# Kernel optimization log

Hardware: AMD Instinct MI355X
Metric: run time of the kernel (lower is better)

The kernel has to match this reference:

```python
import jax, jax.numpy as jnp
import numpy as np

NTYPE = 4
NWAVE = 8
NORBIT = 128
NIPSIN = 3
CUTOFF = 5.0
NEIGH = 64
NB = 32
NATOM = 256
NPAIR_PER = NATOM * NEIGH  # pairs per molecule

# index_para: [0, 1,1,1, 2,...x9] -> length 1 + 3 + 9 = 13
INDEX_PARA = np.concatenate([np.zeros(1, np.int32)] + [np.full(3 ** i, i, np.int32) for i in range(1, NIPSIN)])
NPARA = INDEX_PARA.shape[0]  # 13


def setup_inputs() -> dict:
    key = jax.random.key(0)
    ks = jax.random.split(key, 12)
    cart = jax.random.normal(ks[0], (NB, NATOM, 3), dtype=jnp.float32)
    numatoms = jnp.full((NB,), NATOM, dtype=jnp.int32)
    species = jax.random.randint(ks[1], (NB * NATOM,), 0, NTYPE, dtype=jnp.int32)
    atom_index = jax.random.randint(ks[2], (2, NB, NPAIR_PER), 0, NATOM, dtype=jnp.int32)
    # small nonzero shifts so no pair has exactly zero distance
    shifts = 0.1 * jax.random.normal(ks[3], (NB, NPAIR_PER, 3), dtype=jnp.float32)
    rs = jax.random.uniform(ks[4], (NTYPE, NWAVE), dtype=jnp.float32) * CUTOFF
    inta = -jnp.abs(jax.random.normal(ks[5], (NTYPE, NWAVE), dtype=jnp.float32))
    params = jnp.ones((NTYPE, NWAVE), dtype=jnp.float32) / float(NEIGH)
    hyper = 0.1 * jax.random.normal(ks[6], (NIPSIN, NWAVE, NORBIT), dtype=jnp.float32)
    oc_w0 = 0.05 * jax.random.normal(ks[7], (NORBIT, NWAVE), dtype=jnp.float32)
    oc_e0 = 0.05 * jax.random.normal(ks[8], (NTYPE, NWAVE), dtype=jnp.float32)
    oc_w1 = 0.05 * jax.random.normal(ks[9], (NORBIT, NWAVE), dtype=jnp.float32)
    oc_e1 = 0.05 * jax.random.normal(ks[10], (NTYPE, NWAVE), dtype=jnp.float32)
    return {"cart": cart, "shifts": shifts, "rs": rs, "inta": inta, "params": params,
            "hyper": hyper, "oc_w0": oc_w0, "oc_e0": oc_e0, "oc_w1": oc_w1, "oc_e1": oc_e1,
            "numatoms": numatoms, "species": species, "atom_index": atom_index}


def _angular(dist_vec, f_cut):
    # dist_vec: (N, 3), f_cut: (N,) -> (NPARA, N)
    dv = dist_vec.T  # (3, N)
    ang = f_cut[None, :]  # (1, N)
    parts = [ang]
    for _ in range(1, NIPSIN):
        ang = (ang[:, None, :] * dv[None, :, :]).reshape(-1, ang.shape[-1])
        parts.append(ang)
    return jnp.concatenate(parts, axis=0)  # (13, N)


def reference(cart, shifts, rs, inta, params, hyper, oc_w0, oc_e0, oc_w1, oc_e1,
              numatoms, species, atom_index):
    nbatch, numatom, _ = cart.shape
    totnatom = nbatch * numatom
    # global pair indices: per-molecule neighbor indices + molecule offset
    offsets = jnp.arange(nbatch, dtype=atom_index.dtype) * numatom  # (nbatch,)
    idx12 = (atom_index + offsets[None, :, None]).reshape(2, -1)  # (2, Npair)
    cart_ = cart.reshape(-1, 3)  # (totnatom, 3)
    dist_vec = cart_[idx12[0]] - cart_[idx12[1]] + shifts.reshape(-1, 3)  # (Npair, 3)
    distances = jnp.linalg.norm(dist_vec, axis=-1)  # (Npair,)
    f_cut = jnp.square(0.5 * jnp.cos(distances * (jnp.pi / CUTOFF)) + 0.5)
    sp_pair = species[idx12[1]]  # (Npair,)
    # radial gaussian: exp(inta * (d - rs)^2), per-pair type gather
    radial = jnp.exp(inta[sp_pair] * jnp.square(distances[:, None] - rs[sp_pair]))  # (Npair, nwave)
    ang = _angular(dist_vec, f_cut)  # (NPARA, Npair)
    # orbital[i, j, k] = ang[j, i] * radial[i, k]
    orbital = ang.T[:, :, None] * radial[:, None, :]  # (Npair, NPARA, nwave)
    hyper_exp = hyper[jnp.asarray(INDEX_PARA)]  # (NPARA, nwave, norbit)

    def obtain(orb_coeff):
        worbital = orbital * orb_coeff[idx12[1]][:, None, :]  # gather + scale
        sum_worbital = jax.ops.segment_sum(worbital, idx12[0], num_segments=totnatom)
        hyper_worbital = jnp.einsum('ijk,jkm->ijm', sum_worbital, hyper_exp)
        return jnp.sum(jnp.square(hyper_worbital), axis=1)  # (totnatom, norbit)

    orb_coeff = params[species]  # (totnatom, nwave)
    density = obtain(orb_coeff)
    for w, e in ((oc_w0, oc_e0), (oc_w1, oc_e1)):
        orb_coeff = orb_coeff + jnp.tanh(density @ w + e[species])
        density = obtain(orb_coeff)
    return density
```

## Files before the change

kernel.cpp:

```cpp
#include <hip/hip_runtime.h>
#include <math.h>

#define NTYPE   4
#define NWAVE   8
#define NORBIT  128
#define NEIGH   64
#define NB      32
#define NATOM   256
#define NPP     (NATOM * NEIGH)
#define NPAIR   (NB * NPP)
#define TOTATOM (NB * NATOM)
#define NPARA   13
#define CAP     128

__device__ __forceinline__ float fast_tanh(float x) {
    float ax = fabsf(x);
    float e  = __expf(-2.0f * ax);
    float r  = (1.0f - e) / (1.0f + e);
    return copysignf(r, x);
}

__global__ __launch_bounds__(256) void k_scatter(
    const int* __restrict__ atom_index, const float* __restrict__ cart,
    const float* __restrict__ shifts, const int* __restrict__ species,
    const float* __restrict__ params, const float* __restrict__ rs,
    const float* __restrict__ inta,
    int* __restrict__ cnt, float4* __restrict__ rec,
    float4* __restrict__ radfc, float* __restrict__ coeffA)
{
    const int bl = blockIdx.x, t = threadIdx.x;
    const int b = bl >> 5, c = bl & 31;
    __shared__ float cx[NATOM], cy[NATOM], cz[NATOM];
    __shared__ int   spl[NATOM];
    __shared__ float lrs[NTYPE * NWAVE], lin[NTYPE * NWAVE];
    if (t < NTYPE * NWAVE) { lrs[t] = rs[t]; lin[t] = inta[t]; }
    const int ag = b * NATOM + t;
    cx[t] = cart[ag * 3 + 0];
    cy[t] = cart[ag * 3 + 1];
    cz[t] = cart[ag * 3 + 2];
    spl[t] = species[ag];
    __syncthreads();

    if (c == 0) {
        int sp = spl[t];
#pragma unroll
        for (int w = 0; w < NWAVE; w++) coeffA[ag * NWAVE + w] = params[sp * NWAVE + w];
    }

    const int base = b * NPP + c * 512;
#pragma unroll
    for (int k = 0; k < 2; k++) {
        int p = base + t + k * 256;
        int i = atom_index[p];
        int j = atom_index[NPAIR + p];
        float dx = cx[i] - cx[j] + shifts[p * 3 + 0];
        float dy = cy[i] - cy[j] + shifts[p * 3 + 1];
        float dz = cz[i] - cz[j] + shifts[p * 3 + 2];
        int sp = spl[j];
        float d  = sqrtf(dx * dx + dy * dy + dz * dz);
        float co = __cosf(d * 0.62831853071795864769f);
        float fc = 0.5f * co + 0.5f;
        fc = fc * fc;
        int ig = b * NATOM + i;
        int pos = atomicAdd(&cnt[ig], 1);
        if (pos < CAP) {
            size_t s = (size_t)ig * CAP + pos;
            rec[s] = make_float4(dx, dy, dz, __int_as_float(b * NATOM + j));
            float f[NWAVE];
#pragma unroll
            for (int w = 0; w < NWAVE; w++) {
                float dr = d - lrs[sp * NWAVE + w];
                f[w] = fc * __expf(lin[sp * NWAVE + w] * dr * dr);
            }
            radfc[s * 2 + 0] = make_float4(f[0], f[1], f[2], f[3]);
            radfc[s * 2 + 1] = make_float4(f[4], f[5], f[6], f[7]);
        }
    }
}

__global__ __launch_bounds__(256) void k_pass(
    const float4* __restrict__ rec, const float* __restrict__ radfc,
    const int* __restrict__ cnt, const float* __restrict__ coeff_in,
    const float* __restrict__ hyper, const float* __restrict__ W,
    const float* __restrict__ E, const int* __restrict__ species,
    float* __restrict__ coeff_out, float* __restrict__ density_out, int mode)
{
    const int t = threadIdx.x;
    const int lane = t & 63, wv = t >> 6;
    const int pl = lane >> 3, w = lane & 7;
    const int a = blockIdx.x * 4 + wv;
    __shared__ float lds_S[4][NWAVE * 16];

    int n = cnt[a];
    if (n > CAP) n = CAP;
    const float4* ra = rec + (size_t)a * CAP;
    const float*  rf = radfc + (size_t)a * CAP * 8;

    float S[NPARA];
#pragma unroll
    for (int k = 0; k < NPARA; k++) S[k] = 0.0f;

    int idx = pl;
    float4 r = ra[idx];
    float  f = rf[idx * 8 + w];
    while (idx < n) {
        float4 rn = ra[idx + 8];
        float  fn = rf[(idx + 8) * 8 + w];
        int j = __float_as_int(r.w);
        float cj = coeff_in[j * NWAVE + w];
        float q = f * cj;
        S[0] += q;
        float qx = q * r.x, qy = q * r.y, qz = q * r.z;
        S[1] += qx; S[2] += qy; S[3] += qz;
        S[4]  += qx * r.x; S[5]  += qx * r.y; S[6]  += qx * r.z;
        S[7]  += qy * r.x; S[8]  += qy * r.y; S[9]  += qy * r.z;
        S[10] += qz * r.x; S[11] += qz * r.y; S[12] += qz * r.z;
        idx += 8;
        r = rn;
        f = fn;
    }

#pragma unroll
    for (int k = 0; k < NPARA; k++) {
        S[k] += __shfl_xor(S[k], 8, 64);
        S[k] += __shfl_xor(S[k], 16, 64);
        S[k] += __shfl_xor(S[k], 32, 64);
    }

    if (pl == 0) {
#pragma unroll
        for (int k = 0; k < NPARA; k++) lds_S[wv][w * 16 + k] = S[k];
    }
    __syncthreads();

    const int o0 = lane, o1 = lane + 64;
    float hw0[NPARA], hw1[NPARA];
#pragma unroll
    for (int k = 0; k < NPARA; k++) { hw0[k] = 0.0f; hw1[k] = 0.0f; }
#pragma unroll
    for (int w2 = 0; w2 < NWAVE; w2++) {
        const float* Sw = &lds_S[wv][w2 * 16];
        float4 s0 = *(const float4*)(Sw);
        float4 s1 = *(const float4*)(Sw + 4);
        float4 s2 = *(const float4*)(Sw + 8);
        float  sc = Sw[12];
        float h00 = hyper[w2 * NORBIT + o0];
        float h01 = hyper[w2 * NORBIT + o1];
        float h10 = hyper[(NWAVE + w2) * NORBIT + o0];
        float h11 = hyper[(NWAVE + w2) * NORBIT + o1];
        float h20 = hyper[(2 * NWAVE + w2) * NORBIT + o0];
        float h21 = hyper[(2 * NWAVE + w2) * NORBIT + o1];
        hw0[0]  += s0.x * h00; hw1[0]  += s0.x * h01;
        hw0[1]  += s0.y * h10; hw1[1]  += s0.y * h11;
        hw0[2]  += s0.z * h10; hw1[2]  += s0.z * h11;
        hw0[3]  += s0.w * h10; hw1[3]  += s0.w * h11;
        hw0[4]  += s1.x * h20; hw1[4]  += s1.x * h21;
        hw0[5]  += s1.y * h20; hw1[5]  += s1.y * h21;
        hw0[6]  += s1.z * h20; hw1[6]  += s1.z * h21;
        hw0[7]  += s1.w * h20; hw1[7]  += s1.w * h21;
        hw0[8]  += s2.x * h20; hw1[8]  += s2.x * h21;
        hw0[9]  += s2.y * h20; hw1[9]  += s2.y * h21;
        hw0[10] += s2.z * h20; hw1[10] += s2.z * h21;
        hw0[11] += s2.w * h20; hw1[11] += s2.w * h21;
        hw0[12] += sc   * h20; hw1[12] += sc   * h21;
    }
    float acc0 = 0.0f, acc1 = 0.0f;
#pragma unroll
    for (int k = 0; k < NPARA; k++) {
        acc0 += hw0[k] * hw0[k];
        acc1 += hw1[k] * hw1[k];
    }

    if (mode == 1) {
        density_out[a * NORBIT + o0] = acc0;
        density_out[a * NORBIT + o1] = acc1;
        return;
    }

    float part[NWAVE];
#pragma unroll
    for (int w2 = 0; w2 < NWAVE; w2++)
        part[w2] = acc0 * W[o0 * NWAVE + w2] + acc1 * W[o1 * NWAVE + w2];
#pragma unroll
    for (int mask = 1; mask < 64; mask <<= 1) {
#pragma unroll
        for (int w2 = 0; w2 < NWAVE; w2++)
            part[w2] += __shfl_xor(part[w2], mask, 64);
    }
    if (lane < NWAVE) {
        int sp = species[a];
        coeff_out[a * NWAVE + lane] =
            coeff_in[a * NWAVE + lane] + fast_tanh(part[lane] + E[sp * NWAVE + lane]);
    }
}

extern "C" void kernel_launch(void* const* d_in, const int* in_sizes, int n_in,
                              void* d_out, int out_size, void* d_ws, size_t ws_size,
                              hipStream_t stream) {
    const float* cart    = (const float*)d_in[0];
    const float* shifts  = (const float*)d_in[1];
    const float* rs      = (const float*)d_in[2];
    const float* inta    = (const float*)d_in[3];
    const float* params  = (const float*)d_in[4];
    const float* hyper   = (const float*)d_in[5];
    const float* w0      = (const float*)d_in[6];
    const float* e0      = (const float*)d_in[7];
    const float* w1      = (const float*)d_in[8];
    const float* e1      = (const float*)d_in[9];
    const int* species    = (const int*)d_in[11];
    const int* atom_index = (const int*)d_in[12];
    float* out = (float*)d_out;

    char* ws = (char*)d_ws;
    float4* rec   = (float4*)ws;  ws += (size_t)TOTATOM * CAP * 16;
    float4* radfc = (float4*)ws;  ws += (size_t)TOTATOM * CAP * 32;
    float* coeffA = (float*)ws;   ws += (size_t)TOTATOM * NWAVE * 4;
    float* coeffB = (float*)ws;   ws += (size_t)TOTATOM * NWAVE * 4;
    int* cnt      = (int*)ws;     ws += TOTATOM * 4;

    hipMemsetAsync(cnt, 0, TOTATOM * 4, stream);
    k_scatter<<<1024, 256, 0, stream>>>(atom_index, cart, shifts, species, params,
                                        rs, inta, cnt, rec, radfc, coeffA);
    k_pass<<<TOTATOM / 4, 256, 0, stream>>>(rec, (const float*)radfc, cnt, coeffA,
                                            hyper, w0, e0, species, coeffB, out, 0);
    k_pass<<<TOTATOM / 4, 256, 0, stream>>>(rec, (const float*)radfc, cnt, coeffB,
                                            hyper, w1, e1, species, coeffA, out, 0);
    k_pass<<<TOTATOM / 4, 256, 0, stream>>>(rec, (const float*)radfc, cnt, coeffA,
                                            hyper, w1, e1, species, coeffB, out, 1);
}
```

Before: 165.1 us.

## Fuse scatter and all density passes into one per-molecule kernel

Replaces the global atomic bucketing plus three pass launches with a single kernel where one 1024-thread block handles one molecule. It builds a counting-sort of pairs per center atom in LDS and keeps coefficients, hyper and W weights in LDS. It recomputes radial and cutoff terms in each pass instead of storing them. This removes launch overhead, the memset, the radial buffer and the capacity limit, at the cost of using only 32 blocks on the GPU and redoing transcendental work.

```diff
diff --git a/kernel.cpp b/kernel.cpp
--- a/kernel.cpp
+++ b/kernel.cpp
@@ -4,14 +4,12 @@
 #define NTYPE   4
 #define NWAVE   8
 #define NORBIT  128
-#define NEIGH   64
 #define NB      32
 #define NATOM   256
-#define NPP     (NATOM * NEIGH)
+#define NPP     (NATOM * 64)
 #define NPAIR   (NB * NPP)
 #define TOTATOM (NB * NATOM)
 #define NPARA   13
-#define CAP     128
 
 __device__ __forceinline__ float fast_tanh(float x) {
     float ax = fabsf(x);
@@ -20,178 +18,209 @@
     return copysignf(r, x);
 }
 
-__global__ __launch_bounds__(256) void k_scatter(
+__global__ __launch_bounds__(1024, 1) void k_all(
     const int* __restrict__ atom_index, const float* __restrict__ cart,
     const float* __restrict__ shifts, const int* __restrict__ species,
     const float* __restrict__ params, const float* __restrict__ rs,
-    const float* __restrict__ inta,
-    int* __restrict__ cnt, float4* __restrict__ rec,
-    float4* __restrict__ radfc, float* __restrict__ coeffA)
+    const float* __restrict__ inta, const float* __restrict__ hyper,
+    const float* __restrict__ W0g, const float* __restrict__ E0,
+    const float* __restrict__ W1g, const float* __restrict__ E1,
+    float4* __restrict__ rec, float* __restrict__ out)
 {
-    const int bl = blockIdx.x, t = threadIdx.x;
-    const int b = bl >> 5, c = bl & 31;
+    const int b = blockIdx.x, t = threadIdx.x;
+    const int wave = t >> 6, lane = t & 63;
+    const int pl = lane >> 3, w = lane & 7;
+
+    __shared__ float cA[NATOM * NWAVE];
+    __shared__ float cB[NATOM * NWAVE];
+    __shared__ float sHyp[3 * NWAVE * NORBIT];
+    __shared__ float sW0[NORBIT * NWAVE];
+    __shared__ float sW1[NORBIT * NWAVE];
+    __shared__ float stash[16][NWAVE * 16];
+    __shared__ int   hist[NATOM], cur[NATOM], loffs[NATOM + 1];
     __shared__ float cx[NATOM], cy[NATOM], cz[NATOM];
     __shared__ int   spl[NATOM];
-    __shared__ float lrs[NTYPE * NWAVE], lin[NTYPE * NWAVE];
-    if (t < NTYPE * NWAVE) { lrs[t] = rs[t]; lin[t] = inta[t]; }
-    const int ag = b * NATOM + t;
-    cx[t] = cart[ag * 3 + 0];
-    cy[t] = cart[ag * 3 + 1];
-    cz[t] = cart[ag * 3 + 2];
-    spl[t] = species[ag];
-    __syncthreads();
-
-    if (c == 0) {
-        int sp = spl[t];
-#pragma unroll
-        for (int w = 0; w < NWAVE; w++) coeffA[ag * NWAVE + w] = params[sp * NWAVE + w];
-    }
-
-    const int base = b * NPP + c * 512;
-#pragma unroll
-    for (int k = 0; k < 2; k++) {
-        int p = base + t + k * 256;
-        int i = atom_index[p];
-        int j = atom_index[NPAIR + p];
-        float dx = cx[i] - cx[j] + shifts[p * 3 + 0];
-        float dy = cy[i] - cy[j] + shifts[p * 3 + 1];
-        float dz = cz[i] - cz[j] + shifts[p * 3 + 2];
-        int sp = spl[j];
-        float d  = sqrtf(dx * dx + dy * dy + dz * dz);
-        float co = __cosf(d * 0.62831853071795864769f);
-        float fc = 0.5f * co + 0.5f;
-        fc = fc * fc;
-        int ig = b * NATOM + i;
-        int pos = atomicAdd(&cnt[ig], 1);
-        if (pos < CAP) {
-            size_t s = (size_t)ig * CAP + pos;
-            rec[s] = make_float4(dx, dy, dz, __int_as_float(b * NATOM + j));
-            float f[NWAVE];
-#pragma unroll
-            for (int w = 0; w < NWAVE; w++) {
-                float dr = d - lrs[sp * NWAVE + w];
-                f[w] = fc * __expf(lin[sp * NWAVE + w] * dr * dr);
-            }
-            radfc[s * 2 + 0] = make_float4(f[0], f[1], f[2], f[3]);
-            radfc[s * 2 + 1] = make_float4(f[4], f[5], f[6], f[7]);
+
+    if (t < NATOM) {
+        hist[t] = 0;
+        int ag = b * NATOM + t;
+        cx[t] = cart[ag * 3 + 0];
+        cy[t] = cart[ag * 3 + 1];
+        cz[t] = cart[ag * 3 + 2];
+        spl[t] = species[ag];
+    }
+    for (int e = t; e < 3 * NWAVE * NORBIT; e += 1024) sHyp[e] = hyper[e];
+    for (int e = t; e < NORBIT * NWAVE; e += 1024) { sW0[e] = W0g[e]; sW1[e] = W1g[e]; }
+    __syncthreads();
+
+    for (int e = t; e < NATOM * NWAVE; e += 1024)
+        cA[e] = params[spl[e >> 3] * NWAVE + (e & 7)];
+    int iloc[16];
+    const int base = b * NPP;
+#pragma unroll
+    for (int k = 0; k < 16; k++) {
+        iloc[k] = atom_index[base + t + k * 1024];
+        atomicAdd(&hist[iloc[k]], 1);
+    }
+    __syncthreads();
+
+    if (t < NATOM) cur[t] = hist[t];
+    __syncthreads();
+    for (int d = 1; d < NATOM; d <<= 1) {
+        int v = 0;
+        if (t < NATOM && t >= d) v = cur[t - d];
+        __syncthreads();
+        if (t < NATOM) cur[t] += v;
+        __syncthreads();
+    }
+    if (t < NATOM) {
+        int ex = cur[t] - hist[t];
+        loffs[t] = ex;
+        cur[t] = ex;
+    }
+    if (t == 0) loffs[NATOM] = NPP;
+    __syncthreads();
+
+#pragma unroll
+    for (int k = 0; k < 16; k++) {
+        int p = t + k * 1024;
+        int i = iloc[k];
+        int j = atom_index[NPAIR + base + p];
+        float dx = cx[i] - cx[j] + shifts[(base + p) * 3 + 0];
+        float dy = cy[i] - cy[j] + shifts[(base + p) * 3 + 1];
+        float dz = cz[i] - cz[j] + shifts[(base + p) * 3 + 2];
+        int pos = atomicAdd(&cur[i], 1);
+        rec[base + pos] = make_float4(dx, dy, dz, __int_as_float(j | (spl[j] << 16)));
+    }
+    __syncthreads();
+
+    float rs0 = rs[w],   rs1 = rs[8 + w],   rs2 = rs[16 + w],   rs3 = rs[24 + w];
+    float in0 = inta[w], in1 = inta[8 + w], in2 = inta[16 + w], in3 = inta[24 + w];
+
+    auto pass = [&](const float* cin, float* cout, const float* sW,
+                    const float* Eg, int mode) {
+        for (int ai = wave; ai < NATOM; ai += 16) {
+            const int start = loffs[ai];
+            const int n = loffs[ai + 1] - start;
+            const float4* ra = rec + base + start;
+
+            float S[NPARA];
+#pragma unroll
+            for (int k = 0; k < NPARA; k++) S[k] = 0.0f;
+
+            int idx = pl;
+            float4 r = ra[idx];
+            while (idx < n) {
+                float4 rn = ra[idx + 8];
+                int jp = __float_as_int(r.w);
+                int j  = jp & 0xFFFF;
+                int sp = jp >> 16;
+                float cj = cin[j * NWAVE + w];
+                float d  = sqrtf(r.x * r.x + r.y * r.y + r.z * r.z);
+                float co = __cosf(d * 0.62831853071795864769f);
+                float fc = 0.5f * co + 0.5f;
+                fc = fc * fc;
+                float rw = (sp == 0) ? rs0 : (sp == 1) ? rs1 : (sp == 2) ? rs2 : rs3;
+                float iw = (sp == 0) ? in0 : (sp == 1) ? in1 : (sp == 2) ? in2 : in3;
+                float dr = d - rw;
+                float q  = fc * __expf(iw * dr * dr) * cj;
+                S[0] += q;
+                float qx = q * r.x, qy = q * r.y, qz = q * r.z;
+                S[1] += qx; S[2] += qy; S[3] += qz;
+                S[4]  += qx * r.x; S[5]  += qx * r.y; S[6]  += qx * r.z;
+                S[7]  += qy * r.x; S[8]  += qy * r.y; S[9]  += qy * r.z;
+                S[10] += qz * r.x; S[11] += qz * r.y; S[12] += qz * r.z;
+                idx += 8;
+                r = rn;
+            }
+#pragma unroll
+            for (int k = 0; k < NPARA; k++) {
+                S[k] += __shfl_xor(S[k], 8, 64);
+                S[k] += __shfl_xor(S[k], 16, 64);
+                S[k] += __shfl_xor(S[k], 32, 64);
+            }
+            if (pl == 0) {
+#pragma unroll
+                for (int k = 0; k < NPARA; k++) stash[wave][w * 16 + k] = S[k];
+            }
+
+            const int o0 = lane, o1 = lane + 64;
+            float hw0[NPARA], hw1[NPARA];
+#pragma unroll
+            for (int k = 0; k < NPARA; k++) { hw0[k] = 0.0f; hw1[k] = 0.0f; }
+#pragma unroll
+            for (int w2 = 0; w2 < NWAVE; w2++) {
+                const float* Sw = &stash[wave][w2 * 16];
+                float4 s0 = *(const float4*)(Sw);
+                float4 s1 = *(const float4*)(Sw + 4);
+                float4 s2 = *(const float4*)(Sw + 8);
+                float  sc = Sw[12];
+                float h00 = sHyp[w2 * NORBIT + o0];
+                float h01 = sHyp[w2 * NORBIT + o1];
+                float h10 = sHyp[(NWAVE + w2) * NORBIT + o0];
+                float h11 = sHyp[(NWAVE + w2) * NORBIT + o1];
+                float h20 = sHyp[(2 * NWAVE + w2) * NORBIT + o0];
+                float h21 = sHyp[(2 * NWAVE + w2) * NORBIT + o1];
+                hw0[0]  += s0.x * h00; hw1[0]  += s0.x * h01;
+                hw0[1]  += s0.y * h10; hw1[1]  += s0.y * h11;
+                hw0[2]  += s0.z * h10; hw1[2]  += s0.z * h11;
+                hw0[3]  += s0.w * h10; hw1[3]  += s0.w * h11;
+                hw0[4]  += s1.x * h20; hw1[4]  += s1.x * h21;
+                hw0[5]  += s1.y * h20; hw1[5]  += s1.y * h21;
+                hw0[6]  += s1.z * h20; hw1[6]  += s1.z * h21;
+                hw0[7]  += s1.w * h20; hw1[7]  += s1.w * h21;
+                hw0[8]  += s2.x * h20; hw1[8]  += s2.x * h21;
+                hw0[9]  += s2.y * h20; hw1[9]  += s2.y * h21;
+                hw0[10] += s2.z * h20; hw1[10] += s2.z * h21;
+                hw0[11] += s2.w * h20; hw1[11] += s2.w * h21;
+                hw0[12] += sc   * h20; hw1[12] += sc   * h21;
+            }
+            float acc0 = 0.0f, acc1 = 0.0f;
+#pragma unroll
+            for (int k = 0; k < NPARA; k++) {
+                acc0 += hw0[k] * hw0[k];
+                acc1 += hw1[k] * hw1[k];
+            }
+
+            if (mode == 1) {
+                out[(size_t)(b * NATOM + ai) * NORBIT + o0] = acc0;
+                out[(size_t)(b * NATOM + ai) * NORBIT + o1] = acc1;
+                continue;
+            }
+
+            float part[NWAVE];
+#pragma unroll
+            for (int w2 = 0; w2 < NWAVE; w2++)
+                part[w2] = acc0 * sW[o0 * NWAVE + w2] + acc1 * sW[o1 * NWAVE + w2];
+#pragma unroll
+            for (int m = 1; m <= 4; m <<= 1) {
+#pragma unroll
+                for (int w2 = 0; w2 < NWAVE; w2++)
+                    part[w2] += __shfl_xor(part[w2], m, 64);
+            }
+            float p0 = (lane & 1) ? part[1] : part[0];
+            float p1 = (lane & 1) ? part[3] : part[2];
+            float p2 = (lane & 1) ? part[5] : part[4];
+            float p3 = (lane & 1) ? part[7] : part[6];
+            float q0 = (lane & 2) ? p1 : p0;
+            float q1 = (lane & 2) ? p3 : p2;
+            float v  = (lane & 4) ? q1 : q0;
+            v += __shfl_xor(v, 8, 64);
+            v += __shfl_xor(v, 16, 64);
+            v += __shfl_xor(v, 32, 64);
+            if (lane < NWAVE) {
+                int sp = spl[ai];
+                cout[ai * NWAVE + lane] =
+                    cin[ai * NWAVE + lane] + fast_tanh(v + Eg[sp * NWAVE + lane]);
+            }
         }
-    }
-}
-
-__global__ __launch_bounds__(256) void k_pass(
-    const float4* __restrict__ rec, const float* __restrict__ radfc,
-    const int* __restrict__ cnt, const float* __restrict__ coeff_in,
-    const float* __restrict__ hyper, const float* __restrict__ W,
-    const float* __restrict__ E, const int* __restrict__ species,
-    float* __restrict__ coeff_out, float* __restrict__ density_out, int mode)
-{
-    const int t = threadIdx.x;
-    const int lane = t & 63, wv = t >> 6;
-    const int pl = lane >> 3, w = lane & 7;
-    const int a = blockIdx.x * 4 + wv;
-    __shared__ float lds_S[4][NWAVE * 16];
-
-    int n = cnt[a];
-    if (n > CAP) n = CAP;
-    const float4* ra = rec + (size_t)a * CAP;
-    const float*  rf = radfc + (size_t)a * CAP * 8;
-
-    float S[NPARA];
-#pragma unroll
-    for (int k = 0; k < NPARA; k++) S[k] = 0.0f;
-
-    int idx = pl;
-    float4 r = ra[idx];
-    float  f = rf[idx * 8 + w];
-    while (idx < n) {
-        float4 rn = ra[idx + 8];
-        float  fn = rf[(idx + 8) * 8 + w];
-        int j = __float_as_int(r.w);
-        float cj = coeff_in[j * NWAVE + w];
-        float q = f * cj;
-        S[0] += q;
-        float qx = q * r.x, qy = q * r.y, qz = q * r.z;
-        S[1] += qx; S[2] += qy; S[3] += qz;
-        S[4]  += qx * r.x; S[5]  += qx * r.y; S[6]  += qx * r.z;
-        S[7]  += qy * r.x; S[8]  += qy * r.y; S[9]  += qy * r.z;
-        S[10] += qz * r.x; S[11] += qz * r.y; S[12] += qz * r.z;
-        idx += 8;
-        r = rn;
-        f = fn;
-    }
-
-#pragma unroll
-    for (int k = 0; k < NPARA; k++) {
-        S[k] += __shfl_xor(S[k], 8, 64);
-        S[k] += __shfl_xor(S[k], 16, 64);
-        S[k] += __shfl_xor(S[k], 32, 64);
-    }
-
-    if (pl == 0) {
-#pragma unroll
-        for (int k = 0; k < NPARA; k++) lds_S[wv][w * 16 + k] = S[k];
-    }
-    __syncthreads();
-
-    const int o0 = lane, o1 = lane + 64;
-    float hw0[NPARA], hw1[NPARA];
-#pragma unroll
-    for (int k = 0; k < NPARA; k++) { hw0[k] = 0.0f; hw1[k] = 0.0f; }
-#pragma unroll
-    for (int w2 = 0; w2 < NWAVE; w2++) {
-        const float* Sw = &lds_S[wv][w2 * 16];
-        float4 s0 = *(const float4*)(Sw);
-        float4 s1 = *(const float4*)(Sw + 4);
-        float4 s2 = *(const float4*)(Sw + 8);
-        float  sc = Sw[12];
-        float h00 = hyper[w2 * NORBIT + o0];
-        float h01 = hyper[w2 * NORBIT + o1];
-        float h10 = hyper[(NWAVE + w2) * NORBIT + o0];
-        float h11 = hyper[(NWAVE + w2) * NORBIT + o1];
-        float h20 = hyper[(2 * NWAVE + w2) * NORBIT + o0];
-        float h21 = hyper[(2 * NWAVE + w2) * NORBIT + o1];
-        hw0[0]  += s0.x * h00; hw1[0]  += s0.x * h01;
-        hw0[1]  += s0.y * h10; hw1[1]  += s0.y * h11;
-        hw0[2]  += s0.z * h10; hw1[2]  += s0.z * h11;
-        hw0[3]  += s0.w * h10; hw1[3]  += s0.w * h11;
-        hw0[4]  += s1.x * h20; hw1[4]  += s1.x * h21;
-        hw0[5]  += s1.y * h20; hw1[5]  += s1.y * h21;
-        hw0[6]  += s1.z * h20; hw1[6]  += s1.z * h21;
-        hw0[7]  += s1.w * h20; hw1[7]  += s1.w * h21;
-        hw0[8]  += s2.x * h20; hw1[8]  += s2.x * h21;
-        hw0[9]  += s2.y * h20; hw1[9]  += s2.y * h21;
-        hw0[10] += s2.z * h20; hw1[10] += s2.z * h21;
-        hw0[11] += s2.w * h20; hw1[11] += s2.w * h21;
-        hw0[12] += sc   * h20; hw1[12] += sc   * h21;
-    }
-    float acc0 = 0.0f, acc1 = 0.0f;
-#pragma unroll
-    for (int k = 0; k < NPARA; k++) {
-        acc0 += hw0[k] * hw0[k];
-        acc1 += hw1[k] * hw1[k];
-    }
-
-    if (mode == 1) {
-        density_out[a * NORBIT + o0] = acc0;
-        density_out[a * NORBIT + o1] = acc1;
-        return;
-    }
-
-    float part[NWAVE];
-#pragma unroll
-    for (int w2 = 0; w2 < NWAVE; w2++)
-        part[w2] = acc0 * W[o0 * NWAVE + w2] + acc1 * W[o1 * NWAVE + w2];
-#pragma unroll
-    for (int mask = 1; mask < 64; mask <<= 1) {
-#pragma unroll
-        for (int w2 = 0; w2 < NWAVE; w2++)
-            part[w2] += __shfl_xor(part[w2], mask, 64);
-    }
-    if (lane < NWAVE) {
-        int sp = species[a];
-        coeff_out[a * NWAVE + lane] =
-            coeff_in[a * NWAVE + lane] + fast_tanh(part[lane] + E[sp * NWAVE + lane]);
-    }
+    };
+
+    pass(cA, cB, sW0, E0, 0);
+    __syncthreads();
+    pass(cB, cA, sW1, E1, 0);
+    __syncthreads();
+    pass(cA, nullptr, sW1, E1, 1);
 }
 
 extern "C" void kernel_launch(void* const* d_in, const int* in_sizes, int n_in,
@@ -211,20 +240,8 @@
     const int* atom_index = (const int*)d_in[12];
     float* out = (float*)d_out;
 
-    char* ws = (char*)d_ws;
-    float4* rec   = (float4*)ws;  ws += (size_t)TOTATOM * CAP * 16;
-    float4* radfc = (float4*)ws;  ws += (size_t)TOTATOM * CAP * 32;
-    float* coeffA = (float*)ws;   ws += (size_t)TOTATOM * NWAVE * 4;
-    float* coeffB = (float*)ws;   ws += (size_t)TOTATOM * NWAVE * 4;
-    int* cnt      = (int*)ws;     ws += TOTATOM * 4;
-
-    hipMemsetAsync(cnt, 0, TOTATOM * 4, stream);
-    k_scatter<<<1024, 256, 0, stream>>>(atom_index, cart, shifts, species, params,
-                                        rs, inta, cnt, rec, radfc, coeffA);
-    k_pass<<<TOTATOM / 4, 256, 0, stream>>>(rec, (const float*)radfc, cnt, coeffA,
-                                            hyper, w0, e0, species, coeffB, out, 0);
-    k_pass<<<TOTATOM / 4, 256, 0, stream>>>(rec, (const float*)radfc, cnt, coeffB,
-                                            hyper, w1, e1, species, coeffA, out, 0);
-    k_pass<<<TOTATOM / 4, 256, 0, stream>>>(rec, (const float*)radfc, cnt, coeffA,
-                                            hyper, w1, e1, species, coeffB, out, 1);
+    float4* rec = (float4*)d_ws;
+
+    k_all<<<NB, 1024, 0, stream>>>(atom_index, cart, shifts, species, params,
+                                   rs, inta, hyper, w0, e0, w1, e1, rec, out);
 }
```

New measurement: 451.4 us. 2.73x slower.
